# Kernel tuning notes

Measured on AMD Instinct MI355X. Metric: run time of the kernel, lower is better.

The kernel has to match this reference:

```python
import jax, jax.numpy as jnp
import numpy as np

ROPE_BASE = 10000.0


def _rope_tables(T, d, dtype):
    # inv_freq over even indices, emb = concat(freqs, freqs) -> [T, d]
    inv_freq = 1.0 / (ROPE_BASE ** (jnp.arange(0, d, 2, dtype=jnp.float32) / d))
    t = jnp.arange(T, dtype=jnp.float32)
    freqs = jnp.einsum('i,j->ij', t, inv_freq)          # [T, d/2]
    emb = jnp.concatenate([freqs, freqs], axis=-1)      # [T, d]
    return jnp.cos(emb).astype(dtype), jnp.sin(emb).astype(dtype)


def _rotate_half(x):
    d = x.shape[-1] // 2
    return jnp.concatenate([-x[..., d:], x[..., :d]], axis=-1)


def _apply_rope(x, cos, sin):
    # x: [B, T, H, Dh]; cos/sin: [T, Dh] broadcast over batch and heads
    c = cos[None, :, None, :]
    s = sin[None, :, None, :]
    return x * c + _rotate_half(x) * s


def setup_inputs() -> dict:
    key = jax.random.key(0)
    k1, k2, k3 = jax.random.split(key, 3)
    B, T, C = 2, 2048, 1024
    x = jax.random.normal(k1, (B, T, C), dtype=jnp.float32)
    # weights stored as [in, out] (transposed nn.Linear), scaled like torch init
    W_qkv = jax.random.normal(k2, (C, 3 * C), dtype=jnp.float32) * (C ** -0.5)
    W_proj = jax.random.normal(k3, (C, C), dtype=jnp.float32) * (C ** -0.5)
    return {'x': x, 'W_qkv': W_qkv, 'W_proj': W_proj}


def reference(x, W_qkv, W_proj):
    B, T, C = x.shape
    H = 16
    Dh = C // H
    qkv = x @ W_qkv                                   # [B, T, 3C]
    q, k, v = jnp.split(qkv, 3, axis=-1)
    q = q.reshape(B, T, H, Dh)
    k = k.reshape(B, T, H, Dh)
    v = v.reshape(B, T, H, Dh)
    cos, sin = _rope_tables(T, Dh, x.dtype)
    q = _apply_rope(q, cos, sin)
    k = _apply_rope(k, cos, sin)
    scale = 1.0 / jnp.sqrt(jnp.asarray(Dh, dtype=x.dtype))
    # causal SDPA: scores [B, H, T, T]
    scores = jnp.einsum('bqhd,bkhd->bhqk', q, k) * scale
    causal = jnp.tril(jnp.ones((T, T), dtype=bool))
    scores = jnp.where(causal[None, None], scores, jnp.asarray(-jnp.inf, dtype=scores.dtype))
    attn = jax.nn.softmax(scores, axis=-1)
    y = jnp.einsum('bhqk,bkhd->bqhd', attn, v).reshape(B, T, C)
    return y @ W_proj
```

## Files before the change

### kernel.cpp

```cpp
#include <hip/hip_runtime.h>
#include <cstdint>
#include <cstddef>

typedef __bf16 bf16;
typedef __bf16 bf16x2 __attribute__((ext_vector_type(2)));
typedef __bf16 bf16x4 __attribute__((ext_vector_type(4)));
typedef __bf16 bf16x8 __attribute__((ext_vector_type(8)));
typedef float  f32x4  __attribute__((ext_vector_type(4)));
typedef float  f32x16 __attribute__((ext_vector_type(16)));
typedef int    i32x4  __attribute__((ext_vector_type(4)));

#define G2L(src, dst)                                                          \
  __builtin_amdgcn_global_load_lds(                                            \
      (const __attribute__((address_space(1))) unsigned int*)(src),            \
      (__attribute__((address_space(3))) unsigned int*)(dst), 16, 0, 0)

__global__ void k_f32_to_bf16(const float* __restrict__ in, bf16* __restrict__ out, int n) {
  int i = (blockIdx.x * blockDim.x + threadIdx.x) * 8;
  if (i >= n) return;
  float4 a = *(const float4*)(in + i);
  float4 b = *(const float4*)(in + i + 4);
  bf16x8 o;
  o[0] = (bf16)a.x; o[1] = (bf16)a.y; o[2] = (bf16)a.z; o[3] = (bf16)a.w;
  o[4] = (bf16)b.x; o[5] = (bf16)b.y; o[6] = (bf16)b.z; o[7] = (bf16)b.w;
  *(bf16x8*)(out + i) = o;
}

__global__ void k_transpose_f32_bf16(const float* __restrict__ in, bf16* __restrict__ out,
                                     int R, int C) {
  __shared__ float tile[32][33];
  int c0 = blockIdx.x * 32, r0 = blockIdx.y * 32;
  int tx = threadIdx.x & 31, ty = threadIdx.x >> 5;
#pragma unroll
  for (int i = 0; i < 32; i += 8)
    tile[ty + i][tx] = in[(size_t)(r0 + ty + i) * C + c0 + tx];
  __syncthreads();
#pragma unroll
  for (int i = 0; i < 32; i += 8)
    out[(size_t)(c0 + ty + i) * R + r0 + tx] = (bf16)tile[tx][ty + i];
}

__global__ void k_rope_tables(float* __restrict__ cosT, float* __restrict__ sinT, int total) {
  int i = blockIdx.x * blockDim.x + threadIdx.x;
  if (i >= total) return;
  int t = i >> 5, j = i & 31;
  float inv = powf(10000.0f, -(float)j * (1.0f / 32.0f));
  float f = (float)t * inv;
  cosT[i] = cosf(f);
  sinT[i] = sinf(f);
}

__global__ void k_rope_qk(const bf16* __restrict__ qkv, const float* __restrict__ cosT,
                          const float* __restrict__ sinT, bf16* __restrict__ qr,
                          bf16* __restrict__ kr) {
  int i = blockIdx.x * blockDim.x + threadIdx.x;
  int j = i & 31;
  int h = (i >> 5) & 15;
  int t = (i >> 9) & 2047;
  int b = i >> 20;
  size_t base = (size_t)(b * 2048 + t) * 3072;
  float c = cosT[t * 32 + j], s = sinT[t * 32 + j];
  float qlo = (float)qkv[base + h * 64 + j];
  float qhi = (float)qkv[base + h * 64 + j + 32];
  float klo = (float)qkv[base + 1024 + h * 64 + j];
  float khi = (float)qkv[base + 1024 + h * 64 + j + 32];
  size_t ob = ((size_t)(b * 16 + h) * 2048 + t) * 64;
  qr[ob + j]      = (bf16)((qlo * c - qhi * s) * 0.125f);
  qr[ob + j + 32] = (bf16)((qhi * c + qlo * s) * 0.125f);
  kr[ob + j]      = (bf16)(klo * c - khi * s);
  kr[ob + j + 32] = (bf16)(khi * c + klo * s);
}

__global__ void k_v_scatter(const bf16* __restrict__ qkv, bf16* __restrict__ vt) {
  __shared__ bf16 tile[64][66];
  int bh = blockIdx.y;
  int t0 = blockIdx.x * 64;
  int b = bh >> 4, h = bh & 15;
  int tt = threadIdx.x >> 2, c4 = (threadIdx.x & 3) * 16;
  const bf16* src = qkv + (size_t)(b * 2048 + t0 + tt) * 3072 + 2048 + h * 64 + c4;
  bf16x8 v0 = *(const bf16x8*)src;
  bf16x8 v1 = *(const bf16x8*)(src + 8);
#pragma unroll
  for (int j = 0; j < 8; j++) { tile[tt][c4 + j] = v0[j]; tile[tt][c4 + 8 + j] = v1[j]; }
  __syncthreads();
  int d = threadIdx.x >> 2, tc0 = (threadIdx.x & 3) * 16;
  bf16x8 o0, o1;
#pragma unroll
  for (int j = 0; j < 8; j++) { o0[j] = tile[tc0 + j][d]; o1[j] = tile[tc0 + 8 + j][d]; }
  bf16* dst = vt + ((size_t)bh * 64 + d) * 2048 + t0 + tc0;
  *(bf16x8*)dst = o0;
  *(bf16x8*)(dst + 8) = o1;
}

template <int OUTF32>
__global__ __launch_bounds__(256) void k_gemm_bt(const bf16* __restrict__ A,
                                                 const bf16* __restrict__ Bt,
                                                 float* __restrict__ Cf, bf16* __restrict__ Cb,
                                                 int M, int N, int K) {
  __shared__ __align__(16) bf16 sA[128 * 64];
  __shared__ __align__(16) bf16 sB[128 * 64];
  int m0 = blockIdx.y * 128, n0 = blockIdx.x * 128;
  int t = threadIdx.x, lane = t & 63, w = t >> 6;
  int wr = w >> 1, wc = w & 1;
  int lr = lane & 15, q2 = lane >> 4;
  int srow8 = lane >> 3, pc8 = lane & 7;
  f32x4 acc[4][4] = {};
  for (int k0 = 0; k0 < K; k0 += 64) {
#pragma unroll
    for (int is = 0; is < 4; is++) {
      int r = w * 32 + is * 8 + srow8;
      int lc = pc8 ^ (r & 7);
      G2L(A + (size_t)(m0 + r) * K + k0 + lc * 8, &sA[(w * 32 + is * 8) * 64]);
    }
#pragma unroll
    for (int is = 0; is < 4; is++) {
      int r = w * 32 + is * 8 + srow8;
      int lc = pc8 ^ (r & 7);
      G2L(Bt + (size_t)(n0 + r) * K + k0 + lc * 8, &sB[(w * 32 + is * 8) * 64]);
    }
    __syncthreads();
#pragma unroll
    for (int ch = 0; ch < 2; ch++) {
      bf16x8 af[4], bfr[4];
#pragma unroll
      for (int i = 0; i < 4; i++) {
        int r = wr * 64 + i * 16 + lr;
        af[i] = *(const bf16x8*)&sA[r * 64 + (((ch * 4 + q2) ^ (r & 7)) * 8)];
      }
#pragma unroll
      for (int i = 0; i < 4; i++) {
        int r = wc * 64 + i * 16 + lr;
        bfr[i] = *(const bf16x8*)&sB[r * 64 + (((ch * 4 + q2) ^ (r & 7)) * 8)];
      }
#pragma unroll
      for (int mi = 0; mi < 4; mi++)
#pragma unroll
        for (int ni = 0; ni < 4; ni++)
          acc[mi][ni] = __builtin_amdgcn_mfma_f32_16x16x32_bf16(af[mi], bfr[ni], acc[mi][ni], 0, 0, 0);
    }
    __syncthreads();
  }
  int row_base = m0 + wr * 64, col_base = n0 + wc * 64;
#pragma unroll
  for (int mi = 0; mi < 4; mi++)
#pragma unroll
    for (int ni = 0; ni < 4; ni++) {
      int col = col_base + ni * 16 + lr;
#pragma unroll
      for (int r = 0; r < 4; r++) {
        int row = row_base + mi * 16 + q2 * 4 + r;
        float v = acc[mi][ni][r];
        if (OUTF32) Cf[(size_t)row * N + col] = v;
        else        Cb[(size_t)row * N + col] = (bf16)v;
      }
    }
}

__global__ __launch_bounds__(128) void k_flash_part(const bf16* __restrict__ qr,
                                                    const bf16* __restrict__ kr,
                                                    const bf16* __restrict__ vt,
                                                    bf16* __restrict__ Opart,
                                                    float* __restrict__ ml) {
  const int T = 2048;
  int id = blockIdx.x;
  int slot = id >> 5;
  int bh = id & 31;
  int qt, c;
  if (slot < 8)       { qt = slot; c = 0; }
  else if (slot < 24) { int s = slot - 8;  qt = 8 + (s >> 1);  c = s & 1; }
  else if (slot < 48) { int s = slot - 24; qt = 16 + s / 3;    c = s - (qt - 16) * 3; }
  else                { int s = slot - 48; qt = 24 + (s >> 2); c = s & 3; }
  int kt0 = c * 8;
  int kt1 = qt + 1 < kt0 + 8 ? qt + 1 : kt0 + 8;

  __shared__ __align__(16) bf16 sK[64 * 64];
  __shared__ __align__(16) bf16 sV[64 * 64];
  int t = threadIdx.x, lane = t & 63, w = t >> 6;
  int q31 = lane & 31, hi = lane >> 5;
  int srow8 = lane >> 3, pc8 = lane & 7;

  const bf16* Kbh = kr + (size_t)bh * T * 64;
  const bf16* Vbh = vt + (size_t)bh * 64 * T;

  int qwb = qt * 64 + w * 32;
  int qg = qwb + q31;
  const bf16* qrow = qr + ((size_t)bh * T + qg) * 64 + hi * 8;
  bf16x8 qf[4];
#pragma unroll
  for (int ks = 0; ks < 4; ks++) qf[ks] = *(const bf16x8*)(qrow + ks * 16);
  f32x16 o0 = {}, o1 = {};
  float m = -1e30f, l = 0.f;

  auto stage = [&](int kt) {
#pragma unroll
    for (int is = 0; is < 4; is++) {
      int r = w * 32 + is * 8 + srow8;
      int lc = pc8 ^ (r & 7);
      G2L(Kbh + (size_t)(kt * 64 + r) * 64 + lc * 8, &sK[(w * 32 + is * 8) * 64]);
    }
#pragma unroll
    for (int is = 0; is < 4; is++) {
      int d = w * 32 + is * 8 + srow8;
      int lc = pc8 ^ (d & 7);
      G2L(Vbh + (size_t)d * T + kt * 64 + lc * 8, &sV[(w * 32 + is * 8) * 64]);
    }
  };

  stage(kt0);
  for (int kt = kt0; kt < kt1; kt++) {
    asm volatile("s_waitcnt vmcnt(0)" ::: "memory");
    __builtin_amdgcn_s_barrier();
    asm volatile("" ::: "memory");
    __builtin_amdgcn_sched_barrier(0);
    f32x16 s[2];
    __builtin_amdgcn_s_setprio(1);
#pragma unroll
    for (int kb = 0; kb < 2; kb++) {
      f32x16 a = {};
      int krow = kb * 32 + q31;
#pragma unroll
      for (int ks = 0; ks < 4; ks++) {
        int ch = (ks * 2 + hi) ^ (krow & 7);
        bf16x8 kf = *(const bf16x8*)&sK[krow * 64 + ch * 8];
        a = __builtin_amdgcn_mfma_f32_32x32x16_bf16(kf, qf[ks], a, 0, 0, 0);
      }
      s[kb] = a;
    }
    __builtin_amdgcn_s_setprio(0);
    if (kt == qt) {
      int thr = qg - kt * 64;
#pragma unroll
      for (int kb = 0; kb < 2; kb++)
#pragma unroll
        for (int r = 0; r < 16; r++) {
          int koff = kb * 32 + (r & 3) + 8 * (r >> 2) + 4 * hi;
          if (koff > thr) s[kb][r] = -1e30f;
        }
    }
    float tm[16];
#pragma unroll
    for (int i = 0; i < 16; i++) tm[i] = fmaxf(s[0][i], s[1][i]);
#pragma unroll
    for (int st = 8; st > 0; st >>= 1)
#pragma unroll
      for (int i = 0; i < st; i++) tm[i] = fmaxf(tm[i], tm[i + st]);
    float px = tm[0];
    px = fmaxf(px, __shfl_xor(px, 32, 64));
    float mn = fmaxf(m, px);
    float alpha = __expf(m - mn);
    m = mn;
    float ts[16];
#pragma unroll
    for (int i = 0; i < 16; i++) {
      float p0 = __expf(s[0][i] - m);
      float p1 = __expf(s[1][i] - m);
      s[0][i] = p0;
      s[1][i] = p1;
      ts[i] = p0 + p1;
    }
#pragma unroll
    for (int st = 8; st > 0; st >>= 1)
#pragma unroll
      for (int i = 0; i < st; i++) ts[i] += ts[i + st];
    float rs = ts[0];
    rs += __shfl_xor(rs, 32, 64);
    l = l * alpha + rs;
    int pw[4][4];
#pragma unroll
    for (int kb = 0; kb < 2; kb++) {
      int wd[8];
#pragma unroll
      for (int g = 0; g < 4; g++) {
        bf16x2 a, cc;
        a[0] = (bf16)s[kb][4 * g + 0]; a[1] = (bf16)s[kb][4 * g + 1];
        cc[0] = (bf16)s[kb][4 * g + 2]; cc[1] = (bf16)s[kb][4 * g + 3];
        wd[2 * g]     = __builtin_bit_cast(int, a);
        wd[2 * g + 1] = __builtin_bit_cast(int, cc);
      }
      asm volatile("v_permlane32_swap_b32 %0, %1" : "+v"(wd[0]), "+v"(wd[2]));
      asm volatile("v_permlane32_swap_b32 %0, %1" : "+v"(wd[1]), "+v"(wd[3]));
      asm volatile("v_permlane32_swap_b32 %0, %1" : "+v"(wd[4]), "+v"(wd[6]));
      asm volatile("v_permlane32_swap_b32 %0, %1" : "+v"(wd[5]), "+v"(wd[7]));
      pw[2 * kb][0] = wd[0]; pw[2 * kb][1] = wd[1];
      pw[2 * kb][2] = wd[2]; pw[2 * kb][3] = wd[3];
      pw[2 * kb + 1][0] = wd[4]; pw[2 * kb + 1][1] = wd[5];
      pw[2 * kb + 1][2] = wd[6]; pw[2 * kb + 1][3] = wd[7];
    }
#pragma unroll
    for (int r = 0; r < 16; r++) { o0[r] *= alpha; o1[r] *= alpha; }
    __builtin_amdgcn_s_setprio(1);
#pragma unroll
    for (int ks = 0; ks < 4; ks++) {
      i32x4 pv = {pw[ks][0], pw[ks][1], pw[ks][2], pw[ks][3]};
      bf16x8 pb = __builtin_bit_cast(bf16x8, pv);
      {
        int drow = q31;
        int ch = (ks * 2 + hi) ^ (drow & 7);
        bf16x8 vf = *(const bf16x8*)&sV[drow * 64 + ch * 8];
        o0 = __builtin_amdgcn_mfma_f32_32x32x16_bf16(vf, pb, o0, 0, 0, 0);
      }
      {
        int drow = 32 + q31;
        int ch = (ks * 2 + hi) ^ (drow & 7);
        bf16x8 vf = *(const bf16x8*)&sV[drow * 64 + ch * 8];
        o1 = __builtin_amdgcn_mfma_f32_32x32x16_bf16(vf, pb, o1, 0, 0, 0);
      }
    }
    __builtin_amdgcn_s_setprio(0);
    asm volatile("" ::: "memory");
    __builtin_amdgcn_s_barrier();
    asm volatile("" ::: "memory");
    if (kt + 1 < kt1) stage(kt + 1);
  }
  int qloc = w * 32 + q31;
  bf16* Ob = Opart + (size_t)id * 4096 + qloc * 64;
#pragma unroll
  for (int g = 0; g < 4; g++) {
    bf16x4 v0, v1;
#pragma unroll
    for (int j = 0; j < 4; j++) {
      v0[j] = (bf16)o0[4 * g + j];
      v1[j] = (bf16)o1[4 * g + j];
    }
    *(bf16x4*)&Ob[8 * g + 4 * hi]      = v0;
    *(bf16x4*)&Ob[32 + 8 * g + 4 * hi] = v1;
  }
  if (hi == 0) {
    ml[(size_t)id * 128 + qloc]      = m;
    ml[(size_t)id * 128 + 64 + qloc] = l;
  }
}

__global__ __launch_bounds__(256) void k_combine(const bf16* __restrict__ Opart,
                                                 const float* __restrict__ ml,
                                                 bf16* __restrict__ attn) {
  int bhqt = blockIdx.x;
  int bh = bhqt & 31, qt = bhqt >> 5;
  int b = bh >> 4, h = bh & 15;
  int nch = (qt >> 3) + 1;
  int slot0;
  if (qt < 8)       slot0 = qt;
  else if (qt < 16) slot0 = 8 + (qt - 8) * 2;
  else if (qt < 24) slot0 = 24 + (qt - 16) * 3;
  else              slot0 = 48 + (qt - 24) * 4;
  int t = threadIdx.x;
  int q = t >> 2, ds = (t & 3) * 16;
  float M = -1e30f;
  for (int c = 0; c < nch; c++)
    M = fmaxf(M, ml[(size_t)((slot0 + c) * 32 + bh) * 128 + q]);
  float acc[16] = {};
  float L = 0.f;
  for (int c = 0; c < nch; c++) {
    int p = (slot0 + c) * 32 + bh;
    float wgt = __expf(ml[(size_t)p * 128 + q] - M);
    L += wgt * ml[(size_t)p * 128 + 64 + q];
    const bf16* row = Opart + (size_t)p * 4096 + q * 64 + ds;
    bf16x8 a0 = *(const bf16x8*)row;
    bf16x8 a1 = *(const bf16x8*)(row + 8);
#pragma unroll
    for (int i = 0; i < 8; i++) {
      acc[i]     += wgt * (float)a0[i];
      acc[i + 8] += wgt * (float)a1[i];
    }
  }
  float Linv = 1.0f / L;
  bf16x8 w0, w1;
#pragma unroll
  for (int i = 0; i < 8; i++) {
    w0[i] = (bf16)(acc[i] * Linv);
    w1[i] = (bf16)(acc[i + 8] * Linv);
  }
  bf16* dst = attn + ((size_t)(b * 2048) + qt * 64 + q) * 1024 + h * 64 + ds;
  *(bf16x8*)dst = w0;
  *(bf16x8*)(dst + 8) = w1;
}

extern "C" void kernel_launch(void* const* d_in, const int* in_sizes, int n_in,
                              void* d_out, int out_size, void* d_ws, size_t ws_size,
                              hipStream_t stream) {
  const float* x     = (const float*)d_in[0];
  const float* Wqkv  = (const float*)d_in[1];
  const float* Wproj = (const float*)d_in[2];
  float* outp = (float*)d_out;
  const int B = 2, T = 2048, C = 1024;
  const int M = B * T;

  char* ws = (char*)d_ws;
  size_t off = 0;
  auto alloc = [&](size_t bytes) {
    void* p = ws + off;
    off += (bytes + 255) & ~(size_t)255;
    return p;
  };
  bf16* xb     = (bf16*)alloc((size_t)M * C * 2);
  bf16* wqkvt  = (bf16*)alloc((size_t)3 * C * C * 2);
  bf16* wprojt = (bf16*)alloc((size_t)C * C * 2);
  float* cosT  = (float*)alloc((size_t)T * 32 * 4);
  float* sinT  = (float*)alloc((size_t)T * 32 * 4);
  bf16* qkv    = (bf16*)alloc((size_t)M * 3 * C * 2);
  bf16* qr     = (bf16*)alloc((size_t)M * C * 2);
  bf16* kr     = (bf16*)alloc((size_t)M * C * 2);
  bf16* vt     = (bf16*)alloc((size_t)M * C * 2);
  bf16* attn   = xb;
  bf16* Opart  = qkv;
  float* ml    = (float*)(qkv + (size_t)2560 * 4096);

  k_f32_to_bf16<<<dim3(M * C / 8 / 256), dim3(256), 0, stream>>>(x, xb, M * C);
  k_transpose_f32_bf16<<<dim3(3 * C / 32, C / 32), dim3(256), 0, stream>>>(Wqkv, wqkvt, C, 3 * C);
  k_transpose_f32_bf16<<<dim3(C / 32, C / 32), dim3(256), 0, stream>>>(Wproj, wprojt, C, C);
  k_rope_tables<<<dim3(T * 32 / 256), dim3(256), 0, stream>>>(cosT, sinT, T * 32);
  k_gemm_bt<0><<<dim3(3 * C / 128, M / 128), dim3(256), 0, stream>>>(xb, wqkvt, (float*)nullptr, qkv, M, 3 * C, C);
  k_rope_qk<<<dim3((B * T * 16 * 32) / 256), dim3(256), 0, stream>>>(qkv, cosT, sinT, qr, kr);
  k_v_scatter<<<dim3(T / 64, 32), dim3(256), 0, stream>>>(qkv, vt);
  k_flash_part<<<dim3(2560), dim3(128), 0, stream>>>(qr, kr, vt, Opart, ml);
  k_combine<<<dim3(1024), dim3(256), 0, stream>>>(Opart, ml, attn);
  k_gemm_bt<1><<<dim3(C / 128, M / 128), dim3(256), 0, stream>>>(attn, wprojt, outp, (bf16*)nullptr, M, C, C);
}
```

Baseline: 136.0 us.

## Rebalance flash split-K chunks, use exp2 softmax with lazy rescale, swizzle GEMM blocks

Attention work is now split into chunks of 6 key tiles instead of 8, and the largest query tiles are scheduled first, so more blocks run with more even lengths. The log2(e) factor is folded into the Q scaling so softmax and the combine step can use exp2. The online softmax only rescales O and l when the running max rises by more than a threshold, which skips most rescales. The GEMM block index is remapped across 8 groups to change the cache locality pattern, and the workspace is reordered so ml still fits after the larger partial buffer.

```diff
diff --git a/kernel.cpp b/kernel.cpp
--- a/kernel.cpp
+++ b/kernel.cpp
@@ -65,8 +65,9 @@
   float klo = (float)qkv[base + 1024 + h * 64 + j];
   float khi = (float)qkv[base + 1024 + h * 64 + j + 32];
   size_t ob = ((size_t)(b * 16 + h) * 2048 + t) * 64;
-  qr[ob + j]      = (bf16)((qlo * c - qhi * s) * 0.125f);
-  qr[ob + j + 32] = (bf16)((qhi * c + qlo * s) * 0.125f);
+  const float QS = 0.125f * 1.44269504f;
+  qr[ob + j]      = (bf16)((qlo * c - qhi * s) * QS);
+  qr[ob + j + 32] = (bf16)((qhi * c + qlo * s) * QS);
   kr[ob + j]      = (bf16)(klo * c - khi * s);
   kr[ob + j + 32] = (bf16)(khi * c + klo * s);
 }
@@ -99,7 +100,12 @@
                                                  int M, int N, int K) {
   __shared__ __align__(16) bf16 sA[128 * 64];
   __shared__ __align__(16) bf16 sB[128 * 64];
-  int m0 = blockIdx.y * 128, n0 = blockIdx.x * 128;
+  int nwg = gridDim.x * gridDim.y;
+  int idl = blockIdx.y * gridDim.x + blockIdx.x;
+  int cpx = nwg >> 3;
+  int swz = (idl & 7) * cpx + (idl >> 3);
+  int bx = swz % gridDim.x, by = swz / gridDim.x;
+  int m0 = by * 128, n0 = bx * 128;
   int t = threadIdx.x, lane = t & 63, w = t >> 6;
   int wr = w >> 1, wc = w & 1;
   int lr = lane & 15, q2 = lane >> 4;
@@ -165,13 +171,18 @@
   int id = blockIdx.x;
   int slot = id >> 5;
   int bh = id & 31;
-  int qt, c;
-  if (slot < 8)       { qt = slot; c = 0; }
-  else if (slot < 24) { int s = slot - 8;  qt = 8 + (s >> 1);  c = s & 1; }
-  else if (slot < 48) { int s = slot - 24; qt = 16 + s / 3;    c = s - (qt - 16) * 3; }
-  else                { int s = slot - 48; qt = 24 + (s >> 2); c = s & 3; }
-  int kt0 = c * 8;
-  int kt1 = qt + 1 < kt0 + 8 ? qt + 1 : kt0 + 8;
+  int qt = 31, c = 0;
+  {
+    int s = slot;
+#pragma unroll 1
+    for (int q = 31; q >= 0; --q) {
+      int n = q / 6 + 1;
+      if (s < n) { qt = q; c = s; break; }
+      s -= n;
+    }
+  }
+  int kt0 = c * 6;
+  int kt1 = qt + 1 < kt0 + 6 ? qt + 1 : kt0 + 6;
 
   __shared__ __align__(16) bf16 sK[64 * 64];
   __shared__ __align__(16) bf16 sV[64 * 64];
@@ -246,14 +257,19 @@
       for (int i = 0; i < st; i++) tm[i] = fmaxf(tm[i], tm[i + st]);
     float px = tm[0];
     px = fmaxf(px, __shfl_xor(px, 32, 64));
-    float mn = fmaxf(m, px);
-    float alpha = __expf(m - mn);
-    m = mn;
+    if (__builtin_amdgcn_ballot_w64(px > m + 8.f)) {
+      float mn = fmaxf(m, px);
+      float alpha = exp2f(m - mn);
+      m = mn;
+#pragma unroll
+      for (int r = 0; r < 16; r++) { o0[r] *= alpha; o1[r] *= alpha; }
+      l *= alpha;
+    }
     float ts[16];
 #pragma unroll
     for (int i = 0; i < 16; i++) {
-      float p0 = __expf(s[0][i] - m);
-      float p1 = __expf(s[1][i] - m);
+      float p0 = exp2f(s[0][i] - m);
+      float p1 = exp2f(s[1][i] - m);
       s[0][i] = p0;
       s[1][i] = p1;
       ts[i] = p0 + p1;
@@ -264,7 +280,7 @@
       for (int i = 0; i < st; i++) ts[i] += ts[i + st];
     float rs = ts[0];
     rs += __shfl_xor(rs, 32, 64);
-    l = l * alpha + rs;
+    l += rs;
     int pw[4][4];
 #pragma unroll
     for (int kb = 0; kb < 2; kb++) {
@@ -286,8 +302,6 @@
       pw[2 * kb + 1][0] = wd[4]; pw[2 * kb + 1][1] = wd[5];
       pw[2 * kb + 1][2] = wd[6]; pw[2 * kb + 1][3] = wd[7];
     }
-#pragma unroll
-    for (int r = 0; r < 16; r++) { o0[r] *= alpha; o1[r] *= alpha; }
     __builtin_amdgcn_s_setprio(1);
 #pragma unroll
     for (int ks = 0; ks < 4; ks++) {
@@ -337,12 +351,10 @@
   int bhqt = blockIdx.x;
   int bh = bhqt & 31, qt = bhqt >> 5;
   int b = bh >> 4, h = bh & 15;
-  int nch = (qt >> 3) + 1;
-  int slot0;
-  if (qt < 8)       slot0 = qt;
-  else if (qt < 16) slot0 = 8 + (qt - 8) * 2;
-  else if (qt < 24) slot0 = 24 + (qt - 16) * 3;
-  else              slot0 = 48 + (qt - 24) * 4;
+  int nch = qt / 6 + 1;
+  int slot0 = 0;
+#pragma unroll 1
+  for (int q = 31; q > qt; --q) slot0 += q / 6 + 1;
   int t = threadIdx.x;
   int q = t >> 2, ds = (t & 3) * 16;
   float M = -1e30f;
@@ -352,7 +364,7 @@
   float L = 0.f;
   for (int c = 0; c < nch; c++) {
     int p = (slot0 + c) * 32 + bh;
-    float wgt = __expf(ml[(size_t)p * 128 + q] - M);
+    float wgt = exp2f(ml[(size_t)p * 128 + q] - M);
     L += wgt * ml[(size_t)p * 128 + 64 + q];
     const bf16* row = Opart + (size_t)p * 4096 + q * 64 + ds;
     bf16x8 a0 = *(const bf16x8*)row;
@@ -393,17 +405,17 @@
     return p;
   };
   bf16* xb     = (bf16*)alloc((size_t)M * C * 2);
-  bf16* wqkvt  = (bf16*)alloc((size_t)3 * C * C * 2);
   bf16* wprojt = (bf16*)alloc((size_t)C * C * 2);
   float* cosT  = (float*)alloc((size_t)T * 32 * 4);
   float* sinT  = (float*)alloc((size_t)T * 32 * 4);
   bf16* qkv    = (bf16*)alloc((size_t)M * 3 * C * 2);
+  bf16* wqkvt  = (bf16*)alloc((size_t)3 * C * C * 2);
   bf16* qr     = (bf16*)alloc((size_t)M * C * 2);
   bf16* kr     = (bf16*)alloc((size_t)M * C * 2);
   bf16* vt     = (bf16*)alloc((size_t)M * C * 2);
   bf16* attn   = xb;
   bf16* Opart  = qkv;
-  float* ml    = (float*)(qkv + (size_t)2560 * 4096);
+  float* ml    = (float*)(qkv + (size_t)3264 * 4096);
 
   k_f32_to_bf16<<<dim3(M * C / 8 / 256), dim3(256), 0, stream>>>(x, xb, M * C);
   k_transpose_f32_bf16<<<dim3(3 * C / 32, C / 32), dim3(256), 0, stream>>>(Wqkv, wqkvt, C, 3 * C);
@@ -412,7 +424,7 @@
   k_gemm_bt<0><<<dim3(3 * C / 128, M / 128), dim3(256), 0, stream>>>(xb, wqkvt, (float*)nullptr, qkv, M, 3 * C, C);
   k_rope_qk<<<dim3((B * T * 16 * 32) / 256), dim3(256), 0, stream>>>(qkv, cosT, sinT, qr, kr);
   k_v_scatter<<<dim3(T / 64, 32), dim3(256), 0, stream>>>(qkv, vt);
-  k_flash_part<<<dim3(2560), dim3(128), 0, stream>>>(qr, kr, vt, Opart, ml);
+  k_flash_part<<<dim3(3264), dim3(128), 0, stream>>>(qr, kr, vt, Opart, ml);
   k_combine<<<dim3(1024), dim3(256), 0, stream>>>(Opart, ml, attn);
   k_gemm_bt<1><<<dim3(C / 128, M / 128), dim3(256), 0, stream>>>(attn, wprojt, outp, (bf16*)nullptr, M, C, C);
 }
```

Measured after the change: 142.9 us. 1.05x slower.

## Double-buffer K/V in flash kernel, use exp2 softmax, swizzle GEMM blocks

Applied to the files above, without the earlier changes.

The flash attention kernel now double-buffers the K and V tiles in shared memory, prefetching the next tile before computing on the current one so global loads overlap the MFMA work. Softmax switches from exp to exp2 by folding log2(e) into the query scale applied during RoPE. Flash work items are dispatched in reverse order so the longest causal chunks start first. The GEMM remaps block indices in groups of eight for better L2 locality. Double buffering doubles the LDS use per block, which may lower occupancy.

```diff
diff --git a/kernel.cpp b/kernel.cpp
--- a/kernel.cpp
+++ b/kernel.cpp
@@ -65,8 +65,9 @@
   float klo = (float)qkv[base + 1024 + h * 64 + j];
   float khi = (float)qkv[base + 1024 + h * 64 + j + 32];
   size_t ob = ((size_t)(b * 16 + h) * 2048 + t) * 64;
-  qr[ob + j]      = (bf16)((qlo * c - qhi * s) * 0.125f);
-  qr[ob + j + 32] = (bf16)((qhi * c + qlo * s) * 0.125f);
+  const float QS = 0.125f * 1.44269504f;
+  qr[ob + j]      = (bf16)((qlo * c - qhi * s) * QS);
+  qr[ob + j + 32] = (bf16)((qhi * c + qlo * s) * QS);
   kr[ob + j]      = (bf16)(klo * c - khi * s);
   kr[ob + j + 32] = (bf16)(khi * c + klo * s);
 }
@@ -99,7 +100,12 @@
                                                  int M, int N, int K) {
   __shared__ __align__(16) bf16 sA[128 * 64];
   __shared__ __align__(16) bf16 sB[128 * 64];
-  int m0 = blockIdx.y * 128, n0 = blockIdx.x * 128;
+  int nwg = gridDim.x * gridDim.y;
+  int idl = blockIdx.y * gridDim.x + blockIdx.x;
+  int cpx = nwg >> 3;
+  int swz = (idl & 7) * cpx + (idl >> 3);
+  int bx = swz % gridDim.x, by = swz / gridDim.x;
+  int m0 = by * 128, n0 = bx * 128;
   int t = threadIdx.x, lane = t & 63, w = t >> 6;
   int wr = w >> 1, wc = w & 1;
   int lr = lane & 15, q2 = lane >> 4;
@@ -163,18 +169,18 @@
                                                     float* __restrict__ ml) {
   const int T = 2048;
   int id = blockIdx.x;
-  int slot = id >> 5;
+  int sl = 79 - (id >> 5);
   int bh = id & 31;
   int qt, c;
-  if (slot < 8)       { qt = slot; c = 0; }
-  else if (slot < 24) { int s = slot - 8;  qt = 8 + (s >> 1);  c = s & 1; }
-  else if (slot < 48) { int s = slot - 24; qt = 16 + s / 3;    c = s - (qt - 16) * 3; }
-  else                { int s = slot - 48; qt = 24 + (s >> 2); c = s & 3; }
+  if (sl < 8)       { qt = sl; c = 0; }
+  else if (sl < 24) { int s = sl - 8;  qt = 8 + (s >> 1);  c = s & 1; }
+  else if (sl < 48) { int s = sl - 24; qt = 16 + s / 3;    c = s - (qt - 16) * 3; }
+  else              { int s = sl - 48; qt = 24 + (s >> 2); c = s & 3; }
   int kt0 = c * 8;
   int kt1 = qt + 1 < kt0 + 8 ? qt + 1 : kt0 + 8;
 
-  __shared__ __align__(16) bf16 sK[64 * 64];
-  __shared__ __align__(16) bf16 sV[64 * 64];
+  __shared__ __align__(16) bf16 sK[2][64 * 64];
+  __shared__ __align__(16) bf16 sV[2][64 * 64];
   int t = threadIdx.x, lane = t & 63, w = t >> 6;
   int q31 = lane & 31, hi = lane >> 5;
   int srow8 = lane >> 3, pc8 = lane & 7;
@@ -191,27 +197,35 @@
   f32x16 o0 = {}, o1 = {};
   float m = -1e30f, l = 0.f;
 
-  auto stage = [&](int kt) {
+  auto stage = [&](int buf, int kt) {
 #pragma unroll
     for (int is = 0; is < 4; is++) {
       int r = w * 32 + is * 8 + srow8;
       int lc = pc8 ^ (r & 7);
-      G2L(Kbh + (size_t)(kt * 64 + r) * 64 + lc * 8, &sK[(w * 32 + is * 8) * 64]);
+      G2L(Kbh + (size_t)(kt * 64 + r) * 64 + lc * 8, &sK[buf][(w * 32 + is * 8) * 64]);
     }
 #pragma unroll
     for (int is = 0; is < 4; is++) {
       int d = w * 32 + is * 8 + srow8;
       int lc = pc8 ^ (d & 7);
-      G2L(Vbh + (size_t)d * T + kt * 64 + lc * 8, &sV[(w * 32 + is * 8) * 64]);
+      G2L(Vbh + (size_t)d * T + kt * 64 + lc * 8, &sV[buf][(w * 32 + is * 8) * 64]);
     }
   };
 
-  stage(kt0);
+  stage(0, kt0);
   for (int kt = kt0; kt < kt1; kt++) {
-    asm volatile("s_waitcnt vmcnt(0)" ::: "memory");
+    int buf = (kt - kt0) & 1;
+    if (kt + 1 < kt1) {
+      stage(buf ^ 1, kt + 1);
+      asm volatile("s_waitcnt vmcnt(8)" ::: "memory");
+    } else {
+      asm volatile("s_waitcnt vmcnt(0)" ::: "memory");
+    }
     __builtin_amdgcn_s_barrier();
     asm volatile("" ::: "memory");
     __builtin_amdgcn_sched_barrier(0);
+    const bf16* Kb = &sK[buf][0];
+    const bf16* Vb = &sV[buf][0];
     f32x16 s[2];
     __builtin_amdgcn_s_setprio(1);
 #pragma unroll
@@ -221,7 +235,7 @@
 #pragma unroll
       for (int ks = 0; ks < 4; ks++) {
         int ch = (ks * 2 + hi) ^ (krow & 7);
-        bf16x8 kf = *(const bf16x8*)&sK[krow * 64 + ch * 8];
+        bf16x8 kf = *(const bf16x8*)&Kb[krow * 64 + ch * 8];
         a = __builtin_amdgcn_mfma_f32_32x32x16_bf16(kf, qf[ks], a, 0, 0, 0);
       }
       s[kb] = a;
@@ -247,13 +261,13 @@
     float px = tm[0];
     px = fmaxf(px, __shfl_xor(px, 32, 64));
     float mn = fmaxf(m, px);
-    float alpha = __expf(m - mn);
+    float alpha = exp2f(m - mn);
     m = mn;
     float ts[16];
 #pragma unroll
     for (int i = 0; i < 16; i++) {
-      float p0 = __expf(s[0][i] - m);
-      float p1 = __expf(s[1][i] - m);
+      float p0 = exp2f(s[0][i] - m);
+      float p1 = exp2f(s[1][i] - m);
       s[0][i] = p0;
       s[1][i] = p1;
       ts[i] = p0 + p1;
@@ -296,13 +310,13 @@
       {
         int drow = q31;
         int ch = (ks * 2 + hi) ^ (drow & 7);
-        bf16x8 vf = *(const bf16x8*)&sV[drow * 64 + ch * 8];
+        bf16x8 vf = *(const bf16x8*)&Vb[drow * 64 + ch * 8];
         o0 = __builtin_amdgcn_mfma_f32_32x32x16_bf16(vf, pb, o0, 0, 0, 0);
       }
       {
         int drow = 32 + q31;
         int ch = (ks * 2 + hi) ^ (drow & 7);
-        bf16x8 vf = *(const bf16x8*)&sV[drow * 64 + ch * 8];
+        bf16x8 vf = *(const bf16x8*)&Vb[drow * 64 + ch * 8];
         o1 = __builtin_amdgcn_mfma_f32_32x32x16_bf16(vf, pb, o1, 0, 0, 0);
       }
     }
@@ -310,10 +324,10 @@
     asm volatile("" ::: "memory");
     __builtin_amdgcn_s_barrier();
     asm volatile("" ::: "memory");
-    if (kt + 1 < kt1) stage(kt + 1);
-  }
+  }
+  int pidx = sl * 32 + bh;
   int qloc = w * 32 + q31;
-  bf16* Ob = Opart + (size_t)id * 4096 + qloc * 64;
+  bf16* Ob = Opart + (size_t)pidx * 4096 + qloc * 64;
 #pragma unroll
   for (int g = 0; g < 4; g++) {
     bf16x4 v0, v1;
@@ -326,8 +340,8 @@
     *(bf16x4*)&Ob[32 + 8 * g + 4 * hi] = v1;
   }
   if (hi == 0) {
-    ml[(size_t)id * 128 + qloc]      = m;
-    ml[(size_t)id * 128 + 64 + qloc] = l;
+    ml[(size_t)pidx * 128 + qloc]      = m;
+    ml[(size_t)pidx * 128 + 64 + qloc] = l;
   }
 }
 
@@ -352,7 +366,7 @@
   float L = 0.f;
   for (int c = 0; c < nch; c++) {
     int p = (slot0 + c) * 32 + bh;
-    float wgt = __expf(ml[(size_t)p * 128 + q] - M);
+    float wgt = exp2f(ml[(size_t)p * 128 + q] - M);
     L += wgt * ml[(size_t)p * 128 + 64 + q];
     const bf16* row = Opart + (size_t)p * 4096 + q * 64 + ds;
     bf16x8 a0 = *(const bf16x8*)row;
@@ -393,11 +407,11 @@
     return p;
   };
   bf16* xb     = (bf16*)alloc((size_t)M * C * 2);
-  bf16* wqkvt  = (bf16*)alloc((size_t)3 * C * C * 2);
   bf16* wprojt = (bf16*)alloc((size_t)C * C * 2);
   float* cosT  = (float*)alloc((size_t)T * 32 * 4);
   float* sinT  = (float*)alloc((size_t)T * 32 * 4);
   bf16* qkv    = (bf16*)alloc((size_t)M * 3 * C * 2);
+  bf16* wqkvt  = (bf16*)alloc((size_t)3 * C * C * 2);
   bf16* qr     = (bf16*)alloc((size_t)M * C * 2);
   bf16* kr     = (bf16*)alloc((size_t)M * C * 2);
   bf16* vt     = (bf16*)alloc((size_t)M * C * 2);
```

Result: slower. 148.4 us (+9.1%).
